# Performance work log

Measured on AMD Instinct MI355X. Metric: run time of the kernel, lower is better.

The kernel has to match this reference:

```python
import jax, jax.numpy as jnp
import numpy as np

B, GRID, IN_CO, OUT_CO = 32, 4096, 64, 64
T_EMB, N_MODES = 256, 512
M_HALF = N_MODES // 2 + 1  # 257 retained rFFT modes


def setup_inputs() -> dict:
    key = jax.random.key(0)
    ks = jax.random.split(key, 6)
    w_std = jnp.sqrt(1.0 / (2.0 * IN_CO))
    return {
        "x": jax.random.normal(ks[0], (B, GRID, IN_CO), jnp.float32),
        "t_emb": jax.random.normal(ks[1], (B, T_EMB), jnp.float32),
        "weights_real": jax.random.normal(ks[2], (M_HALF, IN_CO, OUT_CO), jnp.float32) * w_std,
        "weights_imag": jax.random.normal(ks[3], (M_HALF, IN_CO, OUT_CO), jnp.float32) * w_std,
        "dense_real": jax.random.normal(ks[4], (T_EMB, M_HALF), jnp.float32) * jnp.sqrt(1.0 / T_EMB),
        "dense_imag": jax.random.normal(ks[5], (T_EMB, M_HALF), jnp.float32) * jnp.sqrt(1.0 / T_EMB),
    }


def reference(x, t_emb, weights_real, weights_imag, dense_real, dense_imag):
    b, in_grid_sz, _ = x.shape
    m = weights_real.shape[0]  # n_modes//2 + 1
    weights = weights_real + 1j * weights_imag  # (m, in_co, out_co)
    # rFFT over the grid axis
    x_ft = jnp.fft.rfft(x, axis=-2, norm="forward")  # (b, grid//2+1, in_co) complex
    # time modulation per mode: Dense(real) + i*Dense(imag)
    t_tr = (t_emb @ dense_real) + 1j * (t_emb @ dense_imag)  # (b, m)
    # original einsum with eye == elementwise per-mode scale then per-mode matmul
    x_out = jnp.einsum("bmi,mio->bmo", x_ft[:, :m, :], weights) * t_tr[:, :, None]
    out_ft = jnp.zeros((b, in_grid_sz // 2 + 1, weights.shape[-1]), jnp.complex64)
    out_ft = out_ft.at[:, :m, :].set(x_out)
    return jnp.fft.irfft(out_ft, axis=-2, n=in_grid_sz, norm="forward")
```

## Files before the change

kernel.cpp:

```cpp
#include <hip/hip_runtime.h>
#include <hip/hip_bf16.h>

typedef short short8 __attribute__((ext_vector_type(8)));
typedef float f32x4 __attribute__((ext_vector_type(4)));
typedef const void __attribute__((address_space(1))) as1_void;
typedef void __attribute__((address_space(3))) as3_void;

__device__ __forceinline__ float sin_rev(float r) {
  float o; asm("v_sin_f32 %0, %1" : "=v"(o) : "v"(r)); return o;
}
__device__ __forceinline__ float cos_rev(float r) {
  float o; asm("v_cos_f32 %0, %1" : "=v"(o) : "v"(r)); return o;
}

#define INV4096 0.000244140625f
#define INV16   0.0625f

__global__ __launch_bounds__(256) void prep_kernel(__hip_bfloat16* __restrict__ F2,
                                                   __hip_bfloat16* __restrict__ Gm2,
                                                   const float* __restrict__ t_emb,
                                                   const float* __restrict__ dr,
                                                   const float* __restrict__ di,
                                                   float* __restrict__ Sr,
                                                   float* __restrict__ Si,
                                                   const float* __restrict__ x,
                                                   __hip_bfloat16* __restrict__ E,
                                                   __hip_bfloat16* __restrict__ O,
                                                   float* __restrict__ Xr256p,
                                                   float* __restrict__ x2048f) {
  const int bid = blockIdx.x;
  const int tid = threadIdx.x;
  __shared__ float te[256];
  __shared__ float tileA[64][65];
  __shared__ float tileB[64][65];
  __shared__ float red[4][64];
  __shared__ float xm[64];

  if (bid < 512) {
    const int row = bid;
    const int m   = (row < 256) ? row : (row - 255);
    const bool is_cos = (row < 256);
    int n0 = tid * 8;
    union { short8 v; unsigned short u[8]; } pk;
#pragma unroll
    for (int j = 0; j < 8; ++j) {
      int ph = (m * (n0 + j)) & 4095;
      float v = is_cos ?  cos_rev((float)ph * INV4096)
                       : -sin_rev((float)ph * INV4096);
      __hip_bfloat16 h = __float2bfloat16(v);
      pk.u[j] = *(unsigned short*)&h;
    }
    *(short8*)&F2[(size_t)row * 2048 + n0] = pk.v;
  } else if (bid < 1024) {
    const int gb = bid - 512;
    int e  = tid * 8;
    int n  = gb * 4 + (e >> 9);
    int c0 = e & 511;
    union { short8 v; unsigned short u[8]; } pk;
#pragma unroll
    for (int j = 0; j < 8; ++j) {
      int cc = c0 + j;
      int k  = (cc < 256) ? cc : (cc - 255);
      int ph = (n * k) & 4095;
      float v = (cc < 256) ? cos_rev((float)ph * INV4096)
                           : sin_rev((float)ph * INV4096);
      __hip_bfloat16 h = __float2bfloat16(v);
      pk.u[j] = *(unsigned short*)&h;
    }
    *(short8*)&Gm2[(size_t)n * 512 + c0] = pk.v;
  } else if (bid < 1056) {
    int b = bid - 1024;
    te[tid] = t_emb[b * 256 + tid];
    __syncthreads();
    for (int m = tid; m < 257; m += 256) {
      float ar = 0.f, ai = 0.f;
      for (int t = 0; t < 256; ++t) {
        float e = te[t];
        ar += e * dr[t * 257 + m];
        ai += e * di[t * 257 + m];
      }
      float c = (m == 0 ? 1.0f : 2.0f) * (1.0f / 4096.0f);
      Sr[b * 257 + m] = ar * c;
      Si[b * 257 + m] = ai * c;
    }
  } else {
    int idx = bid - 1056;
    int nt = idx & 31;
    int b  = idx >> 5;
    int n0 = nt * 64;
    int m0r = (63 - nt) * 64;
#pragma unroll
    for (int it = 0; it < 4; ++it) {
      int c = it * 256 + tid;
      int r = c >> 4, i4 = (c & 15) * 4;
      float4 v = *(const float4*)&x[((size_t)b * 4096 + n0 + r) * 64 + i4];
      tileA[r][i4 + 0] = v.x; tileA[r][i4 + 1] = v.y;
      tileA[r][i4 + 2] = v.z; tileA[r][i4 + 3] = v.w;
      float4 w = *(const float4*)&x[((size_t)b * 4096 + m0r + r) * 64 + i4];
      tileB[r][i4 + 0] = w.x; tileB[r][i4 + 1] = w.y;
      tileB[r][i4 + 2] = w.z; tileB[r][i4 + 3] = w.w;
    }
    if (tid < 64) xm[tid] = (nt > 0) ? x[((size_t)b * 4096 + (4096 - n0)) * 64 + tid] : 0.f;
    __syncthreads();
#pragma unroll
    for (int it = 0; it < 2; ++it) {
      int c  = it * 256 + tid;
      int i  = c >> 3;
      int ch = c & 7;
      union { short8 v; unsigned short u[8]; } pe, po;
#pragma unroll
      for (int jj = 0; jj < 8; ++jj) {
        int j = ch * 8 + jj;
        float a = tileA[j][i];
        float mir = (j == 0) ? xm[i] : tileB[64 - j][i];
        __hip_bfloat16 he = __float2bfloat16(a + mir);
        __hip_bfloat16 ho = __float2bfloat16(a - mir);
        pe.u[jj] = *(unsigned short*)&he;
        po.u[jj] = *(unsigned short*)&ho;
      }
      size_t base = ((size_t)b * 64 + i) * 2048 + n0 + ch * 8;
      *(short8*)&E[base] = pe.v;
      *(short8*)&O[base] = po.v;
    }
    {
      int i = tid & 63, g = tid >> 6;
      float acc = 0.f;
#pragma unroll
      for (int j = 0; j < 16; ++j) {
        float w = cos_rev((float)j * INV16);
        acc += w * (tileA[g * 16 + j][i] + tileB[g * 16 + j][i]);
      }
      red[g][i] = acc;
    }
    __syncthreads();
    if (tid < 64) {
      Xr256p[((size_t)b * 32 + nt) * 64 + tid] =
          red[0][tid] + red[1][tid] + red[2][tid] + red[3][tid];
      if (nt == 31) x2048f[b * 64 + tid] = tileB[0][tid];
    }
  }
}

template <int NF>
__device__ __forceinline__ void stage_tileT(const __hip_bfloat16* __restrict__ A, int lda, int m0,
                                            const __hip_bfloat16* __restrict__ B, int ldb, int n0,
                                            int kt, __hip_bfloat16* As, __hip_bfloat16* Bs,
                                            int tid) {
#pragma unroll
  for (int j = 0; j < 4; ++j) {
    int c   = j * 256 + tid;
    int row = c >> 3;
    int chg = (c & 7) ^ (row & 7);
    const __hip_bfloat16* ga = A + (size_t)(m0 + row) * lda + kt + chg * 8;
    __hip_bfloat16* la = As + (size_t)(j * 256 + (tid & 192)) * 8;
    __builtin_amdgcn_global_load_lds((as1_void*)ga, (as3_void*)la, 16, 0, 0);
  }
#pragma unroll
  for (int j = 0; j < NF; ++j) {
    int c   = j * 256 + tid;
    int row = c >> 3;
    int chg = (c & 7) ^ (row & 7);
    const __hip_bfloat16* gb = B + (size_t)(n0 + row) * ldb + kt + chg * 8;
    __hip_bfloat16* lb = Bs + (size_t)(j * 256 + (tid & 192)) * 8;
    __builtin_amdgcn_global_load_lds((as1_void*)gb, (as3_void*)lb, 16, 0, 0);
  }
}

template <int NF>
__device__ __forceinline__ void compute_stepT(const __hip_bfloat16* As, const __hip_bfloat16* Bs,
                                              int wr, int wc, int fr, int fq,
                                              f32x4 acc[4][NF]) {
#pragma unroll
  for (int kk = 0; kk < 2; ++kk) {
    short8 av[4], bv[NF];
#pragma unroll
    for (int m = 0; m < 4; ++m) {
      int row  = wr + m * 16 + fr;
      int slot = (fq + kk * 4) ^ (row & 7);
      av[m] = *(const short8*)(As + row * 64 + slot * 8);
    }
#pragma unroll
    for (int n = 0; n < NF; ++n) {
      int row  = wc + n * 16 + fr;
      int slot = (fq + kk * 4) ^ (row & 7);
      bv[n] = *(const short8*)(Bs + row * 64 + slot * 8);
    }
#pragma unroll
    for (int m = 0; m < 4; ++m)
#pragma unroll
      for (int n = 0; n < NF; ++n)
        acc[m][n] = __builtin_amdgcn_mfma_f32_16x16x32_bf16(av[m], bv[n], acc[m][n], 0, 0, 0);
  }
}

template <int NF>
__device__ __forceinline__ void gemm_coreT(const __hip_bfloat16* __restrict__ A, int lda, int m0,
                                           const __hip_bfloat16* __restrict__ B, int ldb, int n0,
                                           int k0, int ksteps,
                                           __hip_bfloat16* As, __hip_bfloat16* Bs,
                                           f32x4 acc[4][NF]) {
  const int tid  = threadIdx.x;
  const int lane = tid & 63;
  const int wv   = tid >> 6;
  const int wr   = (wv >> 1) * 64;
  const int wc   = (wv & 1) * (NF * 16);
  const int fr   = lane & 15;
  const int fq   = lane >> 4;

  for (int ks = 0; ks < ksteps; ++ks) {
    stage_tileT<NF>(A, lda, m0, B, ldb, n0, k0 + ks * 64, As, Bs, tid);
    __syncthreads();
    compute_stepT<NF>(As, Bs, wr, wc, fr, fq, acc);
    __syncthreads();
  }
}

__global__ __launch_bounds__(256) void gemm1_kernel(const __hip_bfloat16* __restrict__ F2,
                                                    const __hip_bfloat16* __restrict__ E,
                                                    const __hip_bfloat16* __restrict__ O,
                                                    __hip_bfloat16* __restrict__ C1,
                                                    int kchunk, int splitk) {
  __shared__ __hip_bfloat16 As[128 * 64];
  __shared__ __hip_bfloat16 Bs[128 * 64];
  int n0 = blockIdx.x * 128;
  int m0 = blockIdx.y * 128;
  int k0 = blockIdx.z * kchunk;
  const __hip_bfloat16* B = (m0 < 256) ? E : O;
  f32x4 acc[4][4];
#pragma unroll
  for (int m = 0; m < 4; ++m)
#pragma unroll
    for (int n = 0; n < 4; ++n)
#pragma unroll
      for (int r = 0; r < 4; ++r) acc[m][n][r] = 0.f;

  gemm_coreT<4>(F2, 2048, m0, B, 2048, n0, k0, kchunk >> 6, As, Bs, acc);

  const int lane = threadIdx.x & 63;
  const int wv   = threadIdx.x >> 6;
  const int wr   = (wv >> 1) * 64, wc = (wv & 1) * 64;
  const int fr   = lane & 15, fq = lane >> 4;
#pragma unroll
  for (int m = 0; m < 4; ++m)
#pragma unroll
    for (int n = 0; n < 4; ++n)
#pragma unroll
      for (int j = 0; j < 4; ++j) {
        int row = m0 + wr + m * 16 + fq * 4 + j;
        int col = n0 + wc + n * 16 + fr;
        C1[((size_t)row * splitk + blockIdx.z) * 2048 + col] = __float2bfloat16(acc[m][n][j]);
      }
}

__global__ __launch_bounds__(256) void mix_kernel(const __hip_bfloat16* __restrict__ C1,
                                                  const float* __restrict__ Xr256p,
                                                  const float* __restrict__ x2048f,
                                                  const float* __restrict__ Wr,
                                                  const float* __restrict__ Wi,
                                                  const float* __restrict__ Sr,
                                                  const float* __restrict__ Si,
                                                  __hip_bfloat16* __restrict__ Y2T,
                                                  __hip_bfloat16* __restrict__ Yx,
                                                  int splitk) {
  const int k = blockIdx.x;
  const int q = blockIdx.y;
  const int tid = threadIdx.x;
  __shared__ float wlr[4096];
  __shared__ float wli[4096];
  __shared__ float xs[2048];

  const float* wrg = Wr + (size_t)k * 4096;
  const float* wig = Wi + (size_t)k * 4096;
  for (int c = tid; c < 1024; c += 256) {
    *(float4*)&wlr[c * 4] = *(const float4*)&wrg[c * 4];
    *(float4*)&wli[c * 4] = *(const float4*)&wig[c * 4];
  }

  {
    const int part = tid >> 7;
    const int ln   = tid & 127;
    const int bi0  = q * 1024 + ln * 8;
    float f[8] = {0.f, 0.f, 0.f, 0.f, 0.f, 0.f, 0.f, 0.f};
    if (part == 0) {
      if (k < 256) {
        const __hip_bfloat16* src = C1 + (size_t)k * splitk * 2048 + bi0;
        for (int z = 0; z < splitk; ++z) {
          short8 v = *(const short8*)(src + (size_t)z * 2048);
#pragma unroll
          for (int j = 0; j < 8; ++j) {
            unsigned short u = (unsigned short)v[j];
            f[j] += __bfloat162float(*(__hip_bfloat16*)&u);
          }
        }
        float par = (k & 1) ? -1.f : 1.f;
#pragma unroll
        for (int j = 0; j < 8; ++j) f[j] += par * x2048f[bi0 + j];
      } else {
        const float* sp = Xr256p + (size_t)(bi0 >> 6) * 2048 + (bi0 & 63);
#pragma unroll 8
        for (int nt = 0; nt < 32; ++nt)
#pragma unroll
          for (int j = 0; j < 8; ++j) f[j] += sp[nt * 64 + j];
      }
    } else if (k > 0) {
      const __hip_bfloat16* src = C1 + (size_t)(255 + k) * splitk * 2048 + bi0;
      for (int z = 0; z < splitk; ++z) {
        short8 v = *(const short8*)(src + (size_t)z * 2048);
#pragma unroll
        for (int j = 0; j < 8; ++j) {
          unsigned short u = (unsigned short)v[j];
          f[j] += __bfloat162float(*(__hip_bfloat16*)&u);
        }
      }
    }
#pragma unroll
    for (int j = 0; j < 8; ++j) xs[part * 1024 + ln * 8 + j] = f[j];
  }
  __syncthreads();

  const int o  = tid & 63;
  const int jj = tid >> 6;
  float pr[4] = {0.f, 0.f, 0.f, 0.f};
  float pi[4] = {0.f, 0.f, 0.f, 0.f};
#pragma unroll 4
  for (int i = 0; i < 64; ++i) {
    float wrv = wlr[i * 64 + o];
    float wiv = wli[i * 64 + o];
#pragma unroll
    for (int u = 0; u < 4; ++u) {
      int lb = (jj * 4 + u) * 64 + i;
      float xr = xs[lb], xi = xs[1024 + lb];
      pr[u] += xr * wrv - xi * wiv;
      pi[u] += xr * wiv + xi * wrv;
    }
  }
#pragma unroll
  for (int u = 0; u < 4; ++u) {
    int b = q * 16 + jj * 4 + u;
    float sr = Sr[b * 257 + k], si = Si[b * 257 + k];
    int bo = b * 64 + o;
    __hip_bfloat16 yr = __float2bfloat16(pr[u] * sr - pi[u] * si);
    __hip_bfloat16 yi = __float2bfloat16(pr[u] * si + pi[u] * sr);
    if (k < 256) Y2T[(size_t)bo * 512 + k] = yr;
    else         Yx[bo] = yr;
    if (k >= 1)  Y2T[(size_t)bo * 512 + 255 + k] = yi;
  }
}

__global__ __launch_bounds__(256) void gemm2_kernel(const __hip_bfloat16* __restrict__ Gm2,
                                                    const __hip_bfloat16* __restrict__ Y2T,
                                                    const __hip_bfloat16* __restrict__ Yx,
                                                    float* __restrict__ out) {
  __shared__ __hip_bfloat16 As[128 * 64];
  __shared__ __hip_bfloat16 Bs[64 * 64];
  __shared__ float red2[4][64];
  int n0 = blockIdx.x * 64;
  int m0 = blockIdx.y * 128;
  f32x4 accC[4][2], accS[4][2];
#pragma unroll
  for (int m = 0; m < 4; ++m)
#pragma unroll
    for (int n = 0; n < 2; ++n)
#pragma unroll
      for (int r = 0; r < 4; ++r) { accC[m][n][r] = 0.f; accS[m][n][r] = 0.f; }

  gemm_coreT<2>(Gm2, 512, m0, Y2T, 512, n0, 0,   4, As, Bs, accC);
  gemm_coreT<2>(Gm2, 512, m0, Y2T, 512, n0, 256, 4, As, Bs, accS);

  const int lane = threadIdx.x & 63;
  const int wv   = threadIdx.x >> 6;
  const int wr   = (wv >> 1) * 64, wc = (wv & 1) * 32;
  const int fr   = lane & 15, fq = lane >> 4;
  float yx[2];
#pragma unroll
  for (int n = 0; n < 2; ++n)
    yx[n] = __bfloat162float(Yx[n0 + wc + n * 16 + fr]);
#pragma unroll
  for (int m = 0; m < 4; ++m)
#pragma unroll
    for (int j = 0; j < 4; ++j) {
      int row = m0 + wr + m * 16 + fq * 4 + j;
      float g = cos_rev((float)(row & 15) * INV16);
#pragma unroll
      for (int n = 0; n < 2; ++n) {
        int col = n0 + wc + n * 16 + fr;
        int b = col >> 6, o = col & 63;
        float vC = accC[m][n][j] + g * yx[n];
        float vS = accS[m][n][j];
        out[((size_t)b * 4096 + row) * 64 + o] = vC - vS;
        if (row > 0)
          out[((size_t)b * 4096 + (4096 - row)) * 64 + o] = vC + vS;
      }
    }

  if (m0 == 0) {
    __syncthreads();
    const int tid = threadIdx.x;
    int col = tid & 63, grp = tid >> 6;
    int bo = n0 + col;
    float s = 0.f;
    for (int k = grp * 64; k < grp * 64 + 64; ++k) {
      float v = __bfloat162float(Y2T[(size_t)bo * 512 + k]);
      s += (k & 1) ? -v : v;
    }
    red2[grp][col] = s;
    __syncthreads();
    if (tid < 64) {
      int bo2 = n0 + tid;
      float alt = red2[0][tid] + red2[1][tid] + red2[2][tid] + red2[3][tid]
                + __bfloat162float(Yx[bo2]);
      int b = bo2 >> 6, o = bo2 & 63;
      out[((size_t)b * 4096 + 2048) * 64 + o] = alt;
    }
  }
}

extern "C" void kernel_launch(void* const* d_in, const int* in_sizes, int n_in,
                              void* d_out, int out_size, void* d_ws, size_t ws_size,
                              hipStream_t stream) {
  const float* x  = (const float*)d_in[0];
  const float* te = (const float*)d_in[1];
  const float* wr = (const float*)d_in[2];
  const float* wi = (const float*)d_in[3];
  const float* dr = (const float*)d_in[4];
  const float* di = (const float*)d_in[5];
  float* out = (float*)d_out;

  char* p = (char*)d_ws;
  auto alloc = [&](size_t bytes) -> char* {
    char* r = p;
    p += (bytes + 255) & ~(size_t)255;
    return r;
  };
  __hip_bfloat16* F2  = (__hip_bfloat16*)alloc(512ull * 2048 * 2);
  __hip_bfloat16* Gm2 = (__hip_bfloat16*)alloc(2048ull * 512 * 2);
  __hip_bfloat16* E   = (__hip_bfloat16*)alloc(2048ull * 2048 * 2);
  __hip_bfloat16* O   = (__hip_bfloat16*)alloc(2048ull * 2048 * 2);
  float* Xr256p = (float*)alloc(32ull * 32 * 64 * 4);
  float* x2048f = (float*)alloc(2048 * 4);
  float* Sr = (float*)alloc(32 * 257 * 4);
  float* Si = (float*)alloc(32 * 257 * 4);
  __hip_bfloat16* Y2T = (__hip_bfloat16*)alloc(2048ull * 512 * 2);
  __hip_bfloat16* Yx  = (__hip_bfloat16*)alloc(2048 * 2);
  size_t fixed = (size_t)(p - (char*)d_ws);

  int splitk = 2;
  if (ws_size >= fixed + 4ull * 512 * 2048 * 2) splitk = 4;
  __hip_bfloat16* C1 = (__hip_bfloat16*)alloc((size_t)splitk * 512 * 2048 * 2);
  int kchunk = 2048 / splitk;

  prep_kernel<<<2080, 256, 0, stream>>>(F2, Gm2, te, dr, di, Sr, Si, x, E, O,
                                        Xr256p, x2048f);
  gemm1_kernel<<<dim3(16, 4, splitk), 256, 0, stream>>>(F2, E, O, C1, kchunk, splitk);
  mix_kernel<<<dim3(257, 2), 256, 0, stream>>>(C1, Xr256p, x2048f, wr, wi, Sr, Si, Y2T, Yx, splitk);
  gemm2_kernel<<<dim3(32, 16), 256, 0, stream>>>(Gm2, Y2T, Yx, out);
}
```

Measured before the change: 85.88 us.

## Generate DFT twiddle tiles on the fly inside GEMM staging instead of precomputing

Removes the precomputed F2 and Gm2 bf16 twiddle matrices from the prep kernel. The GEMM A-tiles are now computed in registers with v_sin/v_cos and written straight to LDS during each k-step, which saves the global write and reread of those matrices and shrinks the prep grid. The cost is extra transcendental and integer ALU work on every staged tile, repeated by every block that shares the same rows. Split-K for gemm1 can also rise to 8 when the workspace allows, giving more parallelism at the price of larger partial buffers for the mix kernel to reduce.

New measurement: 85.54 us. Within noise of the previous version (-0.4%).

```diff
diff --git a/kernel.cpp b/kernel.cpp
--- a/kernel.cpp
+++ b/kernel.cpp
@@ -16,9 +16,7 @@
 #define INV4096 0.000244140625f
 #define INV16   0.0625f
 
-__global__ __launch_bounds__(256) void prep_kernel(__hip_bfloat16* __restrict__ F2,
-                                                   __hip_bfloat16* __restrict__ Gm2,
-                                                   const float* __restrict__ t_emb,
+__global__ __launch_bounds__(256) void prep_kernel(const float* __restrict__ t_emb,
                                                    const float* __restrict__ dr,
                                                    const float* __restrict__ di,
                                                    float* __restrict__ Sr,
@@ -36,40 +34,8 @@
   __shared__ float red[4][64];
   __shared__ float xm[64];
 
-  if (bid < 512) {
-    const int row = bid;
-    const int m   = (row < 256) ? row : (row - 255);
-    const bool is_cos = (row < 256);
-    int n0 = tid * 8;
-    union { short8 v; unsigned short u[8]; } pk;
-#pragma unroll
-    for (int j = 0; j < 8; ++j) {
-      int ph = (m * (n0 + j)) & 4095;
-      float v = is_cos ?  cos_rev((float)ph * INV4096)
-                       : -sin_rev((float)ph * INV4096);
-      __hip_bfloat16 h = __float2bfloat16(v);
-      pk.u[j] = *(unsigned short*)&h;
-    }
-    *(short8*)&F2[(size_t)row * 2048 + n0] = pk.v;
-  } else if (bid < 1024) {
-    const int gb = bid - 512;
-    int e  = tid * 8;
-    int n  = gb * 4 + (e >> 9);
-    int c0 = e & 511;
-    union { short8 v; unsigned short u[8]; } pk;
-#pragma unroll
-    for (int j = 0; j < 8; ++j) {
-      int cc = c0 + j;
-      int k  = (cc < 256) ? cc : (cc - 255);
-      int ph = (n * k) & 4095;
-      float v = (cc < 256) ? cos_rev((float)ph * INV4096)
-                           : sin_rev((float)ph * INV4096);
-      __hip_bfloat16 h = __float2bfloat16(v);
-      pk.u[j] = *(unsigned short*)&h;
-    }
-    *(short8*)&Gm2[(size_t)n * 512 + c0] = pk.v;
-  } else if (bid < 1056) {
-    int b = bid - 1024;
+  if (bid < 32) {
+    int b = bid;
     te[tid] = t_emb[b * 256 + tid];
     __syncthreads();
     for (int m = tid; m < 257; m += 256) {
@@ -84,7 +50,7 @@
       Si[b * 257 + m] = ai * c;
     }
   } else {
-    int idx = bid - 1056;
+    int idx = bid - 32;
     int nt = idx & 31;
     int b  = idx >> 5;
     int n0 = nt * 64;
@@ -141,20 +107,10 @@
   }
 }
 
-template <int NF>
-__device__ __forceinline__ void stage_tileT(const __hip_bfloat16* __restrict__ A, int lda, int m0,
-                                            const __hip_bfloat16* __restrict__ B, int ldb, int n0,
-                                            int kt, __hip_bfloat16* As, __hip_bfloat16* Bs,
-                                            int tid) {
-#pragma unroll
-  for (int j = 0; j < 4; ++j) {
-    int c   = j * 256 + tid;
-    int row = c >> 3;
-    int chg = (c & 7) ^ (row & 7);
-    const __hip_bfloat16* ga = A + (size_t)(m0 + row) * lda + kt + chg * 8;
-    __hip_bfloat16* la = As + (size_t)(j * 256 + (tid & 192)) * 8;
-    __builtin_amdgcn_global_load_lds((as1_void*)ga, (as3_void*)la, 16, 0, 0);
-  }
+template <int NF, int MODE>
+__device__ __forceinline__ void stage_genT(int m0, int kt,
+                                           const __hip_bfloat16* __restrict__ B, int ldb, int n0,
+                                           __hip_bfloat16* As, __hip_bfloat16* Bs, int tid) {
 #pragma unroll
   for (int j = 0; j < NF; ++j) {
     int c   = j * 256 + tid;
@@ -164,6 +120,33 @@
     __hip_bfloat16* lb = Bs + (size_t)(j * 256 + (tid & 192)) * 8;
     __builtin_amdgcn_global_load_lds((as1_void*)gb, (as3_void*)lb, 16, 0, 0);
   }
+#pragma unroll
+  for (int j = 0; j < 4; ++j) {
+    int c   = j * 256 + tid;
+    int row = c >> 3;
+    int chg = (c & 7) ^ (row & 7);
+    int gr  = m0 + row;
+    union { short8 v; unsigned short u[8]; } pk;
+#pragma unroll
+    for (int jj = 0; jj < 8; ++jj) {
+      int col = kt + chg * 8 + jj;
+      float v;
+      if (MODE == 1) {
+        int m  = (gr < 256) ? gr : (gr - 255);
+        int ph = (m * col) & 4095;
+        v = (gr < 256) ?  cos_rev((float)ph * INV4096)
+                       : -sin_rev((float)ph * INV4096);
+      } else {
+        int k  = (col < 256) ? col : (col - 255);
+        int ph = (gr * k) & 4095;
+        v = (col < 256) ? cos_rev((float)ph * INV4096)
+                        : sin_rev((float)ph * INV4096);
+      }
+      __hip_bfloat16 h = __float2bfloat16(v);
+      pk.u[jj] = *(unsigned short*)&h;
+    }
+    *(short8*)&As[(size_t)c * 8] = pk.v;
+  }
 }
 
 template <int NF>
@@ -193,8 +176,8 @@
   }
 }
 
-template <int NF>
-__device__ __forceinline__ void gemm_coreT(const __hip_bfloat16* __restrict__ A, int lda, int m0,
+template <int NF, int MODE>
+__device__ __forceinline__ void gemm_coreT(int m0,
                                            const __hip_bfloat16* __restrict__ B, int ldb, int n0,
                                            int k0, int ksteps,
                                            __hip_bfloat16* As, __hip_bfloat16* Bs,
@@ -208,15 +191,14 @@
   const int fq   = lane >> 4;
 
   for (int ks = 0; ks < ksteps; ++ks) {
-    stage_tileT<NF>(A, lda, m0, B, ldb, n0, k0 + ks * 64, As, Bs, tid);
+    stage_genT<NF, MODE>(m0, k0 + ks * 64, B, ldb, n0, As, Bs, tid);
     __syncthreads();
     compute_stepT<NF>(As, Bs, wr, wc, fr, fq, acc);
     __syncthreads();
   }
 }
 
-__global__ __launch_bounds__(256) void gemm1_kernel(const __hip_bfloat16* __restrict__ F2,
-                                                    const __hip_bfloat16* __restrict__ E,
+__global__ __launch_bounds__(256) void gemm1_kernel(const __hip_bfloat16* __restrict__ E,
                                                     const __hip_bfloat16* __restrict__ O,
                                                     __hip_bfloat16* __restrict__ C1,
                                                     int kchunk, int splitk) {
@@ -234,7 +216,7 @@
 #pragma unroll
       for (int r = 0; r < 4; ++r) acc[m][n][r] = 0.f;
 
-  gemm_coreT<4>(F2, 2048, m0, B, 2048, n0, k0, kchunk >> 6, As, Bs, acc);
+  gemm_coreT<4, 1>(m0, B, 2048, n0, k0, kchunk >> 6, As, Bs, acc);
 
   const int lane = threadIdx.x & 63;
   const int wv   = threadIdx.x >> 6;
@@ -347,8 +329,7 @@
   }
 }
 
-__global__ __launch_bounds__(256) void gemm2_kernel(const __hip_bfloat16* __restrict__ Gm2,
-                                                    const __hip_bfloat16* __restrict__ Y2T,
+__global__ __launch_bounds__(256) void gemm2_kernel(const __hip_bfloat16* __restrict__ Y2T,
                                                     const __hip_bfloat16* __restrict__ Yx,
                                                     float* __restrict__ out) {
   __shared__ __hip_bfloat16 As[128 * 64];
@@ -364,8 +345,8 @@
 #pragma unroll
       for (int r = 0; r < 4; ++r) { accC[m][n][r] = 0.f; accS[m][n][r] = 0.f; }
 
-  gemm_coreT<2>(Gm2, 512, m0, Y2T, 512, n0, 0,   4, As, Bs, accC);
-  gemm_coreT<2>(Gm2, 512, m0, Y2T, 512, n0, 256, 4, As, Bs, accS);
+  gemm_coreT<2, 2>(m0, Y2T, 512, n0, 0,   4, As, Bs, accC);
+  gemm_coreT<2, 2>(m0, Y2T, 512, n0, 256, 4, As, Bs, accS);
 
   const int lane = threadIdx.x & 63;
   const int wv   = threadIdx.x >> 6;
@@ -432,8 +413,6 @@
     p += (bytes + 255) & ~(size_t)255;
     return r;
   };
-  __hip_bfloat16* F2  = (__hip_bfloat16*)alloc(512ull * 2048 * 2);
-  __hip_bfloat16* Gm2 = (__hip_bfloat16*)alloc(2048ull * 512 * 2);
   __hip_bfloat16* E   = (__hip_bfloat16*)alloc(2048ull * 2048 * 2);
   __hip_bfloat16* O   = (__hip_bfloat16*)alloc(2048ull * 2048 * 2);
   float* Xr256p = (float*)alloc(32ull * 32 * 64 * 4);
@@ -445,13 +424,13 @@
   size_t fixed = (size_t)(p - (char*)d_ws);
 
   int splitk = 2;
-  if (ws_size >= fixed + 4ull * 512 * 2048 * 2) splitk = 4;
+  if (ws_size >= fixed + 8ull * 512 * 2048 * 2)      splitk = 8;
+  else if (ws_size >= fixed + 4ull * 512 * 2048 * 2) splitk = 4;
   __hip_bfloat16* C1 = (__hip_bfloat16*)alloc((size_t)splitk * 512 * 2048 * 2);
   int kchunk = 2048 / splitk;
 
-  prep_kernel<<<2080, 256, 0, stream>>>(F2, Gm2, te, dr, di, Sr, Si, x, E, O,
-                                        Xr256p, x2048f);
-  gemm1_kernel<<<dim3(16, 4, splitk), 256, 0, stream>>>(F2, E, O, C1, kchunk, splitk);
+  prep_kernel<<<1056, 256, 0, stream>>>(te, dr, di, Sr, Si, x, E, O, Xr256p, x2048f);
+  gemm1_kernel<<<dim3(16, 4, splitk), 256, 0, stream>>>(E, O, C1, kchunk, splitk);
   mix_kernel<<<dim3(257, 2), 256, 0, stream>>>(C1, Xr256p, x2048f, wr, wi, Sr, Si, Y2T, Yx, splitk);
-  gemm2_kernel<<<dim3(32, 16), 256, 0, stream>>>(Gm2, Y2T, Yx, out);
-}
+  gemm2_kernel<<<dim3(32, 16), 256, 0, stream>>>(Y2T, Yx, out);
+}
```
